# Kernel optimization log

Measured on AMD Instinct MI355X. Metric: run time of the kernel, lower is better.

The kernel has to match this reference:

```python
import jax, jax.numpy as jnp
import numpy as np

B, NN, HL = 64, 64, 50
IN_DIM, POS_DIM, ATT_DIM = 384, 64, 256
NEWS_DIM = IN_DIM + POS_DIM  # 448


def setup_inputs() -> dict:
    key = jax.random.key(0)
    ks = jax.random.split(key, 8)
    pos_emb = jax.random.uniform(ks[3], (100, POS_DIM), jnp.float32, -0.1, 0.1)
    pos_emb = pos_emb.at[0].set(0.0)  # initialize() zeros row 0
    return {
        "log_vec": jax.random.normal(ks[0], (B, HL, IN_DIM), jnp.float32),
        "log_mask": jax.random.randint(ks[1], (B, HL), 0, 2, jnp.int32),
        "news_vec": jax.random.normal(ks[2], (B, NN, IN_DIM), jnp.float32),
        "pos_emb": pos_emb,
        "W1": jax.random.normal(ks[4], (ATT_DIM, 2 * NEWS_DIM), jnp.float32) * 0.02,
        "b1": jnp.zeros((ATT_DIM,), jnp.float32),
        "W2": jax.random.normal(ks[5], (1, ATT_DIM), jnp.float32) * 0.02,
        "b2": jnp.zeros((1,), jnp.float32),
    }


def reference(log_vec, log_mask, news_vec, pos_emb, W1, b1, W2, b2):
    b, nn_ = news_vec.shape[:2]
    hl = log_mask.shape[1]
    # append position embeddings (row 0 for candidates, rows 1..hl for history)
    nf = jnp.concatenate(
        [news_vec, jnp.broadcast_to(pos_emb[0], (b, nn_, POS_DIM))], axis=-1)   # (B,NN,ND)
    lf = jnp.concatenate(
        [log_vec, jnp.broadcast_to(pos_emb[1:hl + 1], (b, hl, POS_DIM))], axis=-1)  # (B,HL,ND)
    # affine1(cat[news, log]) == news @ Wn^T + log @ Wl^T + b1 (avoids concat)
    Wn, Wl = W1[:, :NEWS_DIM], W1[:, NEWS_DIM:]
    pn = jnp.einsum('bnd,ad->bna', nf, Wn)   # (B,NN,A)
    pl = jnp.einsum('bhd,ad->bha', lf, Wl)   # (B,HL,A)
    h = jnp.tanh(pn[:, :, None, :] + pl[:, None, :, :] + b1)  # (B,NN,HL,A)
    logits = jnp.einsum('bnha,a->bnh', h, W2[0]) + b2[0]      # (B,NN,HL)
    logits = jnp.where(log_mask[:, None, :] == 0, jnp.float32(-1e9), logits)
    attn = jax.nn.softmax(logits, axis=2)
    user_log_vecs = jnp.einsum('bnh,bhd->bnd', attn, lf)      # (B,NN,ND)
    return user_log_vecs, nf
```

## Files before the change

### kernel.cpp

```cpp
#include <hip/hip_runtime.h>
#include <math.h>

typedef unsigned short u16;
typedef unsigned int   u32;

#define B_       64
#define NN_      64
#define HL_      50
#define IN_DIM   384
#define POS_DIM  64
#define ATT_DIM  256
#define NEWS_DIM 448

typedef __attribute__((ext_vector_type(8))) short short8;
typedef __attribute__((ext_vector_type(4))) float f32x4;

#if __has_builtin(__builtin_amdgcn_exp2f)
#define EXP2F(x) __builtin_amdgcn_exp2f(x)
#else
#define EXP2F(x) exp2f(x)
#endif
#if __has_builtin(__builtin_amdgcn_rcpf)
#define RCPF(x) __builtin_amdgcn_rcpf(x)
#else
#define RCPF(x) (1.0f/(x))
#endif

__device__ __forceinline__ u16 f2bf(float f) {
    union { float f; u32 i; } v; v.f = f;
    u32 r = v.i + 0x7fffu + ((v.i >> 16) & 1u);
    return (u16)(r >> 16);
}
__device__ __forceinline__ uint2 pack4(float4 v) {
    return make_uint2((u32)f2bf(v.x) | ((u32)f2bf(v.y) << 16),
                      (u32)f2bf(v.z) | ((u32)f2bf(v.w) << 16));
}
__device__ __forceinline__ float fast_tanh(float x) {
    float e = EXP2F(x * 2.88539008f);
    return 1.0f - 2.0f * RCPF(1.0f + e);
}

#define C_W   57344u
#define C_NV  393216u
#define C_LG  307200u
#define C_PS  51200u
#define C_NZ  65536u
#define C_TOT (C_W + C_NV + C_LG + C_PS + C_NZ)

__global__ __launch_bounds__(256) void prep_k(
    const float* __restrict__ W1, const float* __restrict__ newsv,
    const float* __restrict__ logv, const float* __restrict__ pos,
    u16* __restrict__ Wbf, u16* __restrict__ nv_bf, u16* __restrict__ lf_bf,
    float* __restrict__ nf)
{
    u32 i = blockIdx.x * 256u + threadIdx.x;
    if (i < C_W) {
        float4 v = *(const float4*)(W1 + (size_t)i * 4u);
        *(uint2*)(Wbf + (size_t)i * 4u) = pack4(v);
        return;
    }
    i -= C_W;
    if (i < C_NV) {
        float4 v = *(const float4*)(newsv + (size_t)i * 4u);
        *(uint2*)(nv_bf + (size_t)i * 4u) = pack4(v);
        u32 e = i * 4u, r = e / IN_DIM, d = e - r * IN_DIM;
        *(float4*)(nf + (size_t)r * NEWS_DIM + d) = v;
        return;
    }
    i -= C_NV;
    if (i < C_LG) {
        float4 v = *(const float4*)(logv + (size_t)i * 4u);
        u32 e = i * 4u, r = e / IN_DIM, d = e - r * IN_DIM;
        *(uint2*)(lf_bf + (size_t)r * NEWS_DIM + d) = pack4(v);
        return;
    }
    i -= C_LG;
    if (i < C_PS) {
        u32 e = i * 4u, r = e / POS_DIM, d = e - r * POS_DIM;
        u32 h = r % HL_;
        float4 v = *(const float4*)(pos + (size_t)(1u + h) * POS_DIM + d);
        *(uint2*)(lf_bf + (size_t)r * NEWS_DIM + IN_DIM + d) = pack4(v);
        return;
    }
    i -= C_PS;
    if (i < C_NZ) {
        u32 e = i * 4u, r = e / POS_DIM, d = e - r * POS_DIM;
        *(float4*)(nf + (size_t)r * NEWS_DIM + IN_DIM + d) = make_float4(0.f, 0.f, 0.f, 0.f);
    }
}

__global__ __launch_bounds__(64) void gemm_k(
    const u16* __restrict__ nv_bf, const u16* __restrict__ lf_bf,
    const u16* __restrict__ Wbf, const float* __restrict__ b1,
    float* __restrict__ pn, float* __restrict__ plT)
{
    int bid = blockIdx.x;
    int lane = threadIdx.x;
    int m = lane & 15, q = lane >> 4;
    bool is_pn = bid < 256;
    int r0, c0, lda, koff, klen;
    const u16* A;
    if (is_pn) { r0 = (bid & 63) * 64;       c0 = (bid >> 6) * 64; A = nv_bf; lda = IN_DIM;   koff = 0;        klen = IN_DIM; }
    else { int b2 = bid - 256; r0 = (b2 % 50) * 64; c0 = (b2 / 50) * 64; A = lf_bf; lda = NEWS_DIM; koff = NEWS_DIM; klen = NEWS_DIM; }

    f32x4 acc[4][4];
#pragma unroll
    for (int a = 0; a < 4; a++)
#pragma unroll
        for (int b = 0; b < 4; b++) acc[a][b] = (f32x4){0.f, 0.f, 0.f, 0.f};

    const u16* Ap = A + (size_t)(r0 + m) * lda + q * 8;
    const u16* Wp = Wbf + (size_t)(c0 + m) * (2 * NEWS_DIM) + koff + q * 8;

    for (int k = 0; k < klen; k += 32) {
        short8 af[4], wf[4];
#pragma unroll
        for (int rt = 0; rt < 4; rt++) af[rt] = *(const short8*)(Ap + rt * 16 * lda + k);
#pragma unroll
        for (int ct = 0; ct < 4; ct++) wf[ct] = *(const short8*)(Wp + ct * 16 * (2 * NEWS_DIM) + k);
#pragma unroll
        for (int rt = 0; rt < 4; rt++)
#pragma unroll
            for (int ct = 0; ct < 4; ct++)
                acc[rt][ct] = __builtin_amdgcn_mfma_f32_16x16x32_bf16(
                    af[rt], wf[ct], acc[rt][ct], 0, 0, 0);
    }
#pragma unroll
    for (int rt = 0; rt < 4; rt++)
#pragma unroll
        for (int ct = 0; ct < 4; ct++)
#pragma unroll
            for (int i = 0; i < 4; i++) {
                int gr = r0 + rt * 16 + q * 4 + i;
                int gc = c0 + ct * 16 + m;
                float v = acc[rt][ct][i];
                if (is_pn) {
                    pn[(size_t)gr * ATT_DIM + gc] = v + b1[gc];
                } else {
                    int bb = gr / HL_, hh = gr - bb * HL_;
                    plT[(size_t)(bb * ATT_DIM + gc) * HL_ + hh] = v;
                }
            }
}

__global__ __launch_bounds__(256) void attn_k(
    const float* __restrict__ pn, const float* __restrict__ plT,
    const float* __restrict__ w2, const int* __restrict__ lmask,
    float* __restrict__ attn)
{
    int lane = threadIdx.x & 63;
    int wid = (int)(threadIdx.x >> 6);
    int gid = blockIdx.x * 4 + wid;
    int b = gid >> 6;
    int hl = (lane < HL_) ? lane : (HL_ - 1);
    const float* pr = pn + (size_t)gid * ATT_DIM;
    const float* pl = plT + (size_t)b * ATT_DIM * HL_ + hl;
    float acc0 = 0.f, acc1 = 0.f, acc2 = 0.f, acc3 = 0.f;
#pragma unroll 2
    for (int a = 0; a < ATT_DIM; a += 4) {
        float4 p = *(const float4*)(pr + a);
        float4 w = *(const float4*)(w2 + a);
        acc0 = __builtin_fmaf(fast_tanh(p.x + pl[(a + 0) * HL_]), w.x, acc0);
        acc1 = __builtin_fmaf(fast_tanh(p.y + pl[(a + 1) * HL_]), w.y, acc1);
        acc2 = __builtin_fmaf(fast_tanh(p.z + pl[(a + 2) * HL_]), w.z, acc2);
        acc3 = __builtin_fmaf(fast_tanh(p.w + pl[(a + 3) * HL_]), w.w, acc3);
    }
    float acc = (acc0 + acc1) + (acc2 + acc3);
    int mv = (lane < HL_) ? lmask[b * HL_ + lane] : 0;
    float logit = mv ? acc : -1e9f;
    float mx = logit;
#pragma unroll
    for (int o = 32; o > 0; o >>= 1) mx = fmaxf(mx, __shfl_xor(mx, o));
    float e = EXP2F((logit - mx) * 1.44269504f);
    float s = e;
#pragma unroll
    for (int o = 32; o > 0; o >>= 1) s += __shfl_xor(s, o);
    attn[(size_t)gid * 64 + lane] = e * RCPF(s);
}

__global__ __launch_bounds__(256) void out_k(
    const u16* __restrict__ lf_bf, const float* __restrict__ attn,
    float* __restrict__ out)
{
    __shared__ __align__(16) u32 lf_s[HL_ * NEWS_DIM / 2];
    __shared__ float at_s[64];
    int tid = threadIdx.x;
    int b = blockIdx.y, n0 = blockIdx.x * 16;

    const uint4* src = (const uint4*)(lf_bf + (size_t)b * HL_ * NEWS_DIM);
    uint4* dst = (uint4*)lf_s;
    for (int i = tid; i < HL_ * NEWS_DIM / 8; i += 256) dst[i] = src[i];
    __syncthreads();

    for (int ni = 0; ni < 16; ni++) {
        int gid = b * 64 + (n0 + ni);
        if (tid < 64) at_s[tid] = attn[(size_t)gid * 64 + tid];
        __syncthreads();
        if (tid < 224) {
            float a0 = 0.f, a1 = 0.f;
#pragma unroll 5
            for (int h = 0; h < HL_; h++) {
                float av = at_s[h];
                u32 u = lf_s[h * 224 + tid];
                union { u32 i; float f; } lo, hi;
                lo.i = u << 16; hi.i = u & 0xffff0000u;
                a0 = fmaf(av, lo.f, a0);
                a1 = fmaf(av, hi.f, a1);
            }
            float2* orow = (float2*)(out + (size_t)gid * NEWS_DIM);
            orow[tid] = make_float2(a0, a1);
        }
        __syncthreads();
    }
}

extern "C" void kernel_launch(void* const* d_in, const int* in_sizes, int n_in,
                              void* d_out, int out_size, void* d_ws, size_t ws_size,
                              hipStream_t stream) {
    const float* logv  = (const float*)d_in[0];
    const int*   lmask = (const int*)d_in[1];
    const float* newsv = (const float*)d_in[2];
    const float* pos   = (const float*)d_in[3];
    const float* W1    = (const float*)d_in[4];
    const float* b1    = (const float*)d_in[5];
    const float* w2    = (const float*)d_in[6];

    float* out = (float*)d_out;
    float* nf  = out + (size_t)B_ * NN_ * NEWS_DIM;

    char* ws = (char*)d_ws;
    u16*   lf_bf = (u16*)(ws + 0);
    u16*   Wbf   = (u16*)(ws + 2867200);
    u16*   nv_bf = (u16*)(ws + 3325952);
    float* pn    = (float*)(ws + 6471680);
    float* plT   = (float*)(ws + 10665984);
    float* attn  = (float*)(ws + 13942784);

    prep_k<<<(C_TOT + 255) / 256, 256, 0, stream>>>(W1, newsv, logv, pos,
                                                    Wbf, nv_bf, lf_bf, nf);
    gemm_k<<<456, 64, 0, stream>>>(nv_bf, lf_bf, Wbf, b1, pn, plT);
    attn_k<<<B_ * NN_ / 4, 256, 0, stream>>>(pn, plT, w2, lmask, attn);
    out_k <<<dim3(4, B_), 256, 0, stream>>>(lf_bf, attn, out);
}
```

Measured before the change: 146.9 us.

## Compute attention-weighted sum with bf16 MFMA using transposed history features

The weighted-sum stage, previously done with scalar FMAs over a shared-memory copy of the history features, becomes a bf16 MFMA GEMM. The prep kernel now also writes a transposed, zero-padded (to 64) bf16 copy of the history features. The attention kernel stores bf16 probabilities and handles two candidates per wave so each history load is reused twice. The aim is to cut the scalar FMA cost and shared-memory staging in out_k, at the price of scattered 2-byte transposed writes in prep and bf16 rounding of the attention weights.

Result: faster. 137.4 us (-6.4%).

```diff
diff --git a/kernel.cpp b/kernel.cpp
--- a/kernel.cpp
+++ b/kernel.cpp
@@ -45,13 +45,14 @@
 #define C_LG  307200u
 #define C_PS  51200u
 #define C_NZ  65536u
-#define C_TOT (C_W + C_NV + C_LG + C_PS + C_NZ)
+#define C_LTZ 28672u
+#define C_TOT (C_W + C_NV + C_LG + C_PS + C_NZ + C_LTZ)
 
 __global__ __launch_bounds__(256) void prep_k(
     const float* __restrict__ W1, const float* __restrict__ newsv,
     const float* __restrict__ logv, const float* __restrict__ pos,
     u16* __restrict__ Wbf, u16* __restrict__ nv_bf, u16* __restrict__ lf_bf,
-    float* __restrict__ nf)
+    u16* __restrict__ lfT_bf, float* __restrict__ nf)
 {
     u32 i = blockIdx.x * 256u + threadIdx.x;
     if (i < C_W) {
@@ -72,20 +73,34 @@
         float4 v = *(const float4*)(logv + (size_t)i * 4u);
         u32 e = i * 4u, r = e / IN_DIM, d = e - r * IN_DIM;
         *(uint2*)(lf_bf + (size_t)r * NEWS_DIM + d) = pack4(v);
+        u32 b = r / HL_, h = r - b * HL_;
+        u16* t = lfT_bf + ((size_t)b * NEWS_DIM + d) * 64u + h;
+        t[0]   = f2bf(v.x); t[64]  = f2bf(v.y);
+        t[128] = f2bf(v.z); t[192] = f2bf(v.w);
         return;
     }
     i -= C_LG;
     if (i < C_PS) {
         u32 e = i * 4u, r = e / POS_DIM, d = e - r * POS_DIM;
-        u32 h = r % HL_;
+        u32 b = r / HL_, h = r - b * HL_;
         float4 v = *(const float4*)(pos + (size_t)(1u + h) * POS_DIM + d);
         *(uint2*)(lf_bf + (size_t)r * NEWS_DIM + IN_DIM + d) = pack4(v);
+        u16* t = lfT_bf + ((size_t)b * NEWS_DIM + IN_DIM + d) * 64u + h;
+        t[0]   = f2bf(v.x); t[64]  = f2bf(v.y);
+        t[128] = f2bf(v.z); t[192] = f2bf(v.w);
         return;
     }
     i -= C_PS;
     if (i < C_NZ) {
         u32 e = i * 4u, r = e / POS_DIM, d = e - r * POS_DIM;
         *(float4*)(nf + (size_t)r * NEWS_DIM + IN_DIM + d) = make_float4(0.f, 0.f, 0.f, 0.f);
+        return;
+    }
+    i -= C_NZ;
+    if (i < C_LTZ) {
+        u32* t = (u32*)lfT_bf + (size_t)i * 32u + 25u;
+#pragma unroll
+        for (int j = 0; j < 7; j++) t[j] = 0u;
     }
 }
 
@@ -146,71 +161,88 @@
 __global__ __launch_bounds__(256) void attn_k(
     const float* __restrict__ pn, const float* __restrict__ plT,
     const float* __restrict__ w2, const int* __restrict__ lmask,
-    float* __restrict__ attn)
+    u16* __restrict__ attn_bf)
 {
     int lane = threadIdx.x & 63;
-    int wid = (int)(threadIdx.x >> 6);
-    int gid = blockIdx.x * 4 + wid;
-    int b = gid >> 6;
+    int w = (int)(threadIdx.x >> 6);
+    int g = blockIdx.x * 4 + w;
+    int b = g >> 5;
+    int n0 = (g & 31) * 2;
     int hl = (lane < HL_) ? lane : (HL_ - 1);
-    const float* pr = pn + (size_t)gid * ATT_DIM;
+    const float* pr0 = pn + ((size_t)b * NN_ + n0) * ATT_DIM;
+    const float* pr1 = pr0 + ATT_DIM;
     const float* pl = plT + (size_t)b * ATT_DIM * HL_ + hl;
-    float acc0 = 0.f, acc1 = 0.f, acc2 = 0.f, acc3 = 0.f;
+
+    float a00 = 0.f, a01 = 0.f, a10 = 0.f, a11 = 0.f;
 #pragma unroll 2
     for (int a = 0; a < ATT_DIM; a += 4) {
-        float4 p = *(const float4*)(pr + a);
-        float4 w = *(const float4*)(w2 + a);
-        acc0 = __builtin_fmaf(fast_tanh(p.x + pl[(a + 0) * HL_]), w.x, acc0);
-        acc1 = __builtin_fmaf(fast_tanh(p.y + pl[(a + 1) * HL_]), w.y, acc1);
-        acc2 = __builtin_fmaf(fast_tanh(p.z + pl[(a + 2) * HL_]), w.z, acc2);
-        acc3 = __builtin_fmaf(fast_tanh(p.w + pl[(a + 3) * HL_]), w.w, acc3);
-    }
-    float acc = (acc0 + acc1) + (acc2 + acc3);
+        float4 w4 = *(const float4*)(w2 + a);
+        float4 p0 = *(const float4*)(pr0 + a);
+        float4 p1 = *(const float4*)(pr1 + a);
+        float l0 = pl[(a + 0) * HL_];
+        float l1 = pl[(a + 1) * HL_];
+        float l2 = pl[(a + 2) * HL_];
+        float l3 = pl[(a + 3) * HL_];
+        a00 = __builtin_fmaf(fast_tanh(p0.x + l0), w4.x, a00);
+        a10 = __builtin_fmaf(fast_tanh(p1.x + l0), w4.x, a10);
+        a01 = __builtin_fmaf(fast_tanh(p0.y + l1), w4.y, a01);
+        a11 = __builtin_fmaf(fast_tanh(p1.y + l1), w4.y, a11);
+        a00 = __builtin_fmaf(fast_tanh(p0.z + l2), w4.z, a00);
+        a10 = __builtin_fmaf(fast_tanh(p1.z + l2), w4.z, a10);
+        a01 = __builtin_fmaf(fast_tanh(p0.w + l3), w4.w, a01);
+        a11 = __builtin_fmaf(fast_tanh(p1.w + l3), w4.w, a11);
+    }
+    float acc0 = a00 + a01, acc1 = a10 + a11;
     int mv = (lane < HL_) ? lmask[b * HL_ + lane] : 0;
-    float logit = mv ? acc : -1e9f;
-    float mx = logit;
-#pragma unroll
-    for (int o = 32; o > 0; o >>= 1) mx = fmaxf(mx, __shfl_xor(mx, o));
-    float e = EXP2F((logit - mx) * 1.44269504f);
-    float s = e;
-#pragma unroll
-    for (int o = 32; o > 0; o >>= 1) s += __shfl_xor(s, o);
-    attn[(size_t)gid * 64 + lane] = e * RCPF(s);
+    float lg0 = mv ? acc0 : -1e9f;
+    float lg1 = mv ? acc1 : -1e9f;
+    float mx0 = lg0, mx1 = lg1;
+#pragma unroll
+    for (int o = 32; o > 0; o >>= 1) {
+        mx0 = fmaxf(mx0, __shfl_xor(mx0, o));
+        mx1 = fmaxf(mx1, __shfl_xor(mx1, o));
+    }
+    float e0 = EXP2F((lg0 - mx0) * 1.44269504f);
+    float e1 = EXP2F((lg1 - mx1) * 1.44269504f);
+    float s0 = e0, s1 = e1;
+#pragma unroll
+    for (int o = 32; o > 0; o >>= 1) {
+        s0 += __shfl_xor(s0, o);
+        s1 += __shfl_xor(s1, o);
+    }
+    u16* ab = attn_bf + (size_t)b * (NN_ * 64) + (size_t)n0 * 64 + lane;
+    ab[0]  = f2bf(e0 * RCPF(s0));
+    ab[64] = f2bf(e1 * RCPF(s1));
 }
 
 __global__ __launch_bounds__(256) void out_k(
-    const u16* __restrict__ lf_bf, const float* __restrict__ attn,
+    const u16* __restrict__ attn_bf, const u16* __restrict__ lfT_bf,
     float* __restrict__ out)
 {
-    __shared__ __align__(16) u32 lf_s[HL_ * NEWS_DIM / 2];
-    __shared__ float at_s[64];
-    int tid = threadIdx.x;
-    int b = blockIdx.y, n0 = blockIdx.x * 16;
-
-    const uint4* src = (const uint4*)(lf_bf + (size_t)b * HL_ * NEWS_DIM);
-    uint4* dst = (uint4*)lf_s;
-    for (int i = tid; i < HL_ * NEWS_DIM / 8; i += 256) dst[i] = src[i];
-    __syncthreads();
-
-    for (int ni = 0; ni < 16; ni++) {
-        int gid = b * 64 + (n0 + ni);
-        if (tid < 64) at_s[tid] = attn[(size_t)gid * 64 + tid];
-        __syncthreads();
-        if (tid < 224) {
-            float a0 = 0.f, a1 = 0.f;
-#pragma unroll 5
-            for (int h = 0; h < HL_; h++) {
-                float av = at_s[h];
-                u32 u = lf_s[h * 224 + tid];
-                union { u32 i; float f; } lo, hi;
-                lo.i = u << 16; hi.i = u & 0xffff0000u;
-                a0 = fmaf(av, lo.f, a0);
-                a1 = fmaf(av, hi.f, a1);
-            }
-            float2* orow = (float2*)(out + (size_t)gid * NEWS_DIM);
-            orow[tid] = make_float2(a0, a1);
-        }
-        __syncthreads();
+    int bid = blockIdx.x;
+    int b = bid >> 2, quad = bid & 3;
+    int w = (int)(threadIdx.x >> 6);
+    int lane = threadIdx.x & 63;
+    int m = lane & 15, q = lane >> 4;
+    int n0 = w * 16;
+
+    const u16* Ap = attn_bf + (size_t)b * (NN_ * 64) + (size_t)(n0 + m) * 64 + q * 8;
+    short8 a0 = *(const short8*)(Ap);
+    short8 a1 = *(const short8*)(Ap + 32);
+    const u16* Bb = lfT_bf + (size_t)b * NEWS_DIM * 64;
+
+#pragma unroll
+    for (int dt = 0; dt < 7; dt++) {
+        int d0 = quad * 112 + dt * 16;
+        const u16* Bp = Bb + (size_t)(d0 + m) * 64 + q * 8;
+        short8 b0 = *(const short8*)(Bp);
+        short8 b1 = *(const short8*)(Bp + 32);
+        f32x4 c = (f32x4){0.f, 0.f, 0.f, 0.f};
+        c = __builtin_amdgcn_mfma_f32_16x16x32_bf16(a0, b0, c, 0, 0, 0);
+        c = __builtin_amdgcn_mfma_f32_16x16x32_bf16(a1, b1, c, 0, 0, 0);
+#pragma unroll
+        for (int i = 0; i < 4; i++)
+            out[((size_t)b * NN_ + n0 + q * 4 + i) * NEWS_DIM + d0 + m] = c[i];
     }
 }
 
@@ -229,16 +261,17 @@
     float* nf  = out + (size_t)B_ * NN_ * NEWS_DIM;
 
     char* ws = (char*)d_ws;
-    u16*   lf_bf = (u16*)(ws + 0);
-    u16*   Wbf   = (u16*)(ws + 2867200);
-    u16*   nv_bf = (u16*)(ws + 3325952);
-    float* pn    = (float*)(ws + 6471680);
-    float* plT   = (float*)(ws + 10665984);
-    float* attn  = (float*)(ws + 13942784);
-
-    prep_k<<<(C_TOT + 255) / 256, 256, 0, stream>>>(W1, newsv, logv, pos,
-                                                    Wbf, nv_bf, lf_bf, nf);
+    u16*   lf_bf   = (u16*)(ws + 0);
+    u16*   Wbf     = (u16*)(ws + 2867200);
+    u16*   nv_bf   = (u16*)(ws + 3325952);
+    float* pn      = (float*)(ws + 6471680);
+    float* plT     = (float*)(ws + 10665984);
+    u16*   lfT_bf  = (u16*)(ws + 13942784);
+    u16*   attn_bf = (u16*)(ws + 17612800);
+
+    prep_k<<<C_TOT / 256, 256, 0, stream>>>(W1, newsv, logv, pos,
+                                            Wbf, nv_bf, lf_bf, lfT_bf, nf);
     gemm_k<<<456, 64, 0, stream>>>(nv_bf, lf_bf, Wbf, b1, pn, plT);
-    attn_k<<<B_ * NN_ / 4, 256, 0, stream>>>(pn, plT, w2, lmask, attn);
-    out_k <<<dim3(4, B_), 256, 0, stream>>>(lf_bf, attn, out);
-}
+    attn_k<<<512, 256, 0, stream>>>(pn, plT, w2, lmask, attn_bf);
+    out_k <<<256, 256, 0, stream>>>(attn_bf, lfT_bf, out);
+}
```
